# Kernel optimization log

Hardware: AMD Instinct MI355X
Metric: run time of the kernel (lower is better)

## Reference

```python
import jax, jax.numpy as jnp
import numpy as np


def silu(v):
    return v * jax.nn.sigmoid(v)


def setup_inputs() -> dict:
    key = jax.random.key(0)
    ks = jax.random.split(key, 9)
    B, L, d_model = 2, 2048, 1024
    expand, d_state, d_conv = 2, 16, 4
    d_inner = expand * d_model          # 2048
    dt_rank = (d_model + 15) // 16      # 64 (ceil(d_model/16))
    sc = 0.02
    s = lambda k, shape: (jax.random.normal(k, shape, jnp.float32) * sc)
    A_init = jnp.tile(jnp.arange(1, d_state + 1, dtype=jnp.float32), (d_inner, 1))
    return {
        "x": jax.random.normal(ks[0], (B, L, d_model), jnp.float32),
        "in_proj_w": s(ks[1], (2 * d_inner, d_model)),
        "conv_w": s(ks[2], (d_inner, 1, d_conv)),
        "conv_b": s(ks[3], (d_inner,)),
        "x_proj_w": s(ks[4], (dt_rank + 2 * d_state, d_inner)),
        "dt_proj_w": s(ks[5], (d_inner, dt_rank)),
        "dt_proj_b": s(ks[6], (d_inner,)),
        "A_log": jnp.log(A_init),
        "D": jnp.ones((d_inner,), jnp.float32),
        "out_proj_w": s(ks[7], (d_model, d_inner)),
    }


def _mamba(x, in_proj_w, conv_w, conv_b, x_proj_w, dt_proj_w, dt_proj_b, A_log, D, out_proj_w):
    Bsz, L, d_model = x.shape
    d_inner, _, d_conv = conv_w.shape
    d_state = A_log.shape[1]
    dt_rank = dt_proj_w.shape[1]

    # input projection -> [B, L, 2*d_inner], split into conv branch and gate
    xz = jnp.einsum('bld,ed->ble', x, in_proj_w)
    x_in, z = jnp.split(xz, 2, axis=-1)

    # causal depthwise conv1d over sequence
    xt = jnp.transpose(x_in, (0, 2, 1))                      # [B, d_inner, L]
    xt = jnp.pad(xt, ((0, 0), (0, 0), (d_conv - 1, 0)))
    xc = jax.lax.conv_general_dilated(
        xt, conv_w, window_strides=(1,), padding='VALID',
        dimension_numbers=('NCH', 'OIH', 'NCH'),
        feature_group_count=d_inner)
    xc = xc + conv_b[None, :, None]
    u = silu(jnp.transpose(xc, (0, 2, 1)))                   # [B, L, d_inner]

    # ssm parameter projections
    x_dbl = jnp.einsum('ble,fe->blf', u, x_proj_w)           # [B, L, dt_rank + 2*d_state]
    dt, B_ssm, C_ssm = jnp.split(x_dbl, [dt_rank, dt_rank + d_state], axis=-1)
    delta = jax.nn.softplus(jnp.einsum('blr,er->ble', dt, dt_proj_w) + dt_proj_b)  # [B,L,d_inner]
    A = -jnp.exp(A_log)                                       # [d_inner, d_state]

    # selective scan: h_t = exp(delta_t * A) * h_{t-1} + delta_t * u_t * B_t
    def step(h, inp):
        d_t, B_t, C_t, u_t = inp                              # [B,e],[B,n],[B,n],[B,e]
        dA = jnp.exp(d_t[..., None] * A)                      # [B, d_inner, d_state]
        h = dA * h + (d_t * u_t)[..., None] * B_t[:, None, :]
        y = jnp.einsum('ben,bn->be', h, C_t)
        return h, y

    h0 = jnp.zeros((Bsz, d_inner, d_state), x.dtype)
    scan_in = (jnp.swapaxes(delta, 0, 1), jnp.swapaxes(B_ssm, 0, 1),
               jnp.swapaxes(C_ssm, 0, 1), jnp.swapaxes(u, 0, 1))
    _, ys = jax.lax.scan(step, h0, scan_in)                   # ys: [L, B, d_inner]
    y = jnp.swapaxes(ys, 0, 1) + u * D                        # skip term D*u

    y = y * silu(z)                                           # gate
    return jnp.einsum('ble,de->bld', y, out_proj_w)


def reference(x, in_proj_w, conv_w, conv_b, x_proj_w, dt_proj_w, dt_proj_b, A_log, D, out_proj_w):
    # ResidualMamba: x + Mamba(x)
    return x + _mamba(x, in_proj_w, conv_w, conv_b, x_proj_w,
                      dt_proj_w, dt_proj_b, A_log, D, out_proj_w)
```

## Files before the change

kernel.cpp:

```cpp
#include <hip/hip_runtime.h>
#include <hip/hip_bf16.h>
#include <math.h>

typedef __bf16 bf16;
typedef __attribute__((ext_vector_type(8))) __bf16 bf16x8;
typedef __attribute__((ext_vector_type(4))) __bf16 bf16x4;
typedef __attribute__((ext_vector_type(4))) float  f32x4;

static constexpr int Bsz = 2, L = 2048, DM = 1024, DI = 2048, DS = 16, DTR = 64;
static constexpr int M   = Bsz * L;
static constexpr int NXZ = 2 * DI;
static constexpr int NXD = DTR + 2 * DS;
static constexpr int NC  = 32;
static constexpr int CL  = L / NC;
static constexpr int KS  = 8;
static constexpr float LOG2E = 1.4426950408889634f;

__device__ inline float ex2(float x) { return __builtin_amdgcn_exp2f(x); }

__device__ inline void gload_lds16(const void* g, void* l)
{
    __builtin_amdgcn_global_load_lds(
        (const __attribute__((address_space(1))) void*)g,
        (__attribute__((address_space(3))) void*)l, 16, 0, 0);
}

#define SBAR() { asm volatile("" ::: "memory"); __builtin_amdgcn_s_barrier(); asm volatile("" ::: "memory"); }
#define VMCNT4() asm volatile("s_waitcnt vmcnt(4)" ::: "memory")
#define VMCNT3() asm volatile("s_waitcnt vmcnt(3)" ::: "memory")
#define VMCNT0() asm volatile("s_waitcnt vmcnt(0)" ::: "memory")


static constexpr int C0 = M * DM / 4;
static constexpr int C1 = C0 + NXZ * DM / 4;
static constexpr int C2 = C1 + DM * DI / 4;
static constexpr int C3 = C2 + NXD * DI / 4;
static constexpr int C4 = C3 + DI * DTR / 4;

__global__ __launch_bounds__(256)
void cast_all(const float* __restrict__ s0, const float* __restrict__ s1,
              const float* __restrict__ s2, const float* __restrict__ s3,
              const float* __restrict__ s4,
              bf16* __restrict__ d0, bf16* __restrict__ d1,
              bf16* __restrict__ d2, bf16* __restrict__ d3,
              bf16* __restrict__ d4)
{
    const int i = blockIdx.x * 256 + threadIdx.x;
    const float* s; bf16* d; int off;
    if      (i < C0) { s = s0; d = d0; off = 0;  }
    else if (i < C1) { s = s1; d = d1; off = C0; }
    else if (i < C2) { s = s2; d = d2; off = C1; }
    else if (i < C3) { s = s3; d = d3; off = C2; }
    else             { s = s4; d = d4; off = C3; }
    const int j = i - off;
    float4 v = ((const float4*)s)[j];
    bf16x4 o = {(bf16)v.x, (bf16)v.y, (bf16)v.z, (bf16)v.w};
    ((bf16x4*)d)[j] = o;
}

static constexpr int GK  = DM;
static constexpr int GNT = GK / 64;

__device__ __forceinline__ void stage_half(const bf16* __restrict__ Gbase, int ld,
                                           int kbase, bf16* lds_slot, int tid, int wid)
{
    const int rl = tid >> 2;
    const int ks = ((((tid & 3) - ((tid >> 3) & 3)) & 3) << 3);
#pragma unroll
    for (int i = 0; i < 2; ++i)
        gload_lds16(Gbase + (size_t)(i * 128 + rl) * ld + kbase + ks,
                    lds_slot + i * 4096 + wid * 512);
}

template<int MH>
__device__ __forceinline__ void ldA4(const bf16* As, int abase, bf16x8 af[4])
{
#pragma unroll
    for (int mm = 0; mm < 4; ++mm)
        af[mm] = *(const bf16x8*)(As + abase + (MH * 4 + mm) * 512);
}

__device__ __forceinline__ void ldB4(const bf16* Bs, int bbase, bf16x8 bfr[4])
{
#pragma unroll
    for (int nn = 0; nn < 4; ++nn)
        bfr[nn] = *(const bf16x8*)(Bs + bbase + nn * 512);
}

template<int MH>
__device__ __forceinline__ void mfma16(f32x4 acc[8][4], const bf16x8 af[4],
                                       const bf16x8 bfr[4])
{
#pragma unroll
    for (int mm = 0; mm < 4; ++mm)
#pragma unroll
        for (int nn = 0; nn < 4; ++nn)
            acc[MH * 4 + mm][nn] = __builtin_amdgcn_mfma_f32_16x16x32_bf16(
                af[mm], bfr[nn], acc[MH * 4 + mm][nn], 0, 0, 0);
}

__global__ __launch_bounds__(512, 1)
void gemm256_inproj(const bf16* __restrict__ A, const bf16* __restrict__ Bw,
                    bf16* __restrict__ C)
{
    __shared__ __align__(16) bf16 Asl[4 * 8192];
    __shared__ __align__(16) bf16 Bsl[4 * 8192];

    const int tid  = threadIdx.x;
    const int wid  = tid >> 6;
    const int lane = tid & 63;
    const int wr   = wid >> 2;
    const int wc   = wid & 3;
    const int fr   = lane & 15;
    const int ko16 = lane >> 4;
    const int kx   = (((ko16 + ((fr >> 1) & 3)) & 3) << 3);

    const int bid = blockIdx.x;
    const int wg  = (bid & 7) * 32 + (bid >> 3);
    const int by  = wg >> 4, bx = wg & 15;
    const int row0 = by * 256, col0 = bx * 256;

    const bf16* Ablk = A  + (size_t)row0 * GK;
    const bf16* Bblk = Bw + (size_t)col0 * GK;

    const int abase = (wr * 128 + fr) * 32 + kx;
    const int bbase = (wc * 64 + fr) * 32 + kx;

    f32x4 acc[8][4] = {};
    bf16x8 af[4], bfr[4];

    stage_half(Ablk, GK, 0,       Asl + 0 * 8192, tid, wid);
    stage_half(Bblk, GK, 0,       Bsl + 0 * 8192, tid, wid);
    stage_half(Ablk, GK, 32,      Asl + 1 * 8192, tid, wid);
    stage_half(Bblk, GK, 32,      Bsl + 1 * 8192, tid, wid);
    stage_half(Ablk, GK, 64,      Asl + 2 * 8192, tid, wid);
    stage_half(Bblk, GK, 64,      Bsl + 2 * 8192, tid, wid);
    VMCNT4();
    SBAR();

    for (int t = 0; t < GNT; ++t) {
        const int sk0 = (2 * t) & 3, sk1 = (2 * t + 1) & 3;
        const bf16* As0 = Asl + sk0 * 8192;
        const bf16* As1 = Asl + sk1 * 8192;
        const bf16* Bs0 = Bsl + sk0 * 8192;
        const bf16* Bs1 = Bsl + sk1 * 8192;

        ldA4<0>(As0, abase, af);
        ldB4(Bs0, bbase, bfr);
        if (t + 1 < GNT)
            stage_half(Ablk, GK, (t + 1) * 64 + 32, Asl + ((2 * t + 3) & 3) * 8192, tid, wid);
        SBAR();
        __builtin_amdgcn_s_setprio(1);
        mfma16<0>(acc, af, bfr);
        __builtin_amdgcn_s_setprio(0);
        SBAR();

        ldA4<1>(As0, abase, af);
        if (t + 1 < GNT)
            stage_half(Bblk, GK, (t + 1) * 64 + 32, Bsl + ((2 * t + 3) & 3) * 8192, tid, wid);
        SBAR();
        __builtin_amdgcn_s_setprio(1);
        mfma16<1>(acc, af, bfr);
        __builtin_amdgcn_s_setprio(0);
        SBAR();

        ldA4<0>(As1, abase, af);
        ldB4(Bs1, bbase, bfr);
        if (t + 2 < GNT)
            stage_half(Ablk, GK, (t + 2) * 64, Asl + sk0 * 8192, tid, wid);
        SBAR();
        __builtin_amdgcn_s_setprio(1);
        mfma16<0>(acc, af, bfr);
        __builtin_amdgcn_s_setprio(0);
        SBAR();

        ldA4<1>(As1, abase, af);
        if (t + 2 < GNT)
            stage_half(Bblk, GK, (t + 2) * 64, Bsl + sk0 * 8192, tid, wid);
        SBAR();
        __builtin_amdgcn_s_setprio(1);
        mfma16<1>(acc, af, bfr);
        __builtin_amdgcn_s_setprio(0);
        if (t < GNT - 3) { VMCNT4(); } else { VMCNT0(); }
        SBAR();
    }

    const int r0 = row0 + wr * 128 + (ko16 << 2);
    const int c0 = col0 + wc * 64 + fr;
#pragma unroll
    for (int m = 0; m < 8; ++m)
#pragma unroll
        for (int n = 0; n < 4; ++n)
#pragma unroll
            for (int r = 0; r < 4; ++r)
                C[(size_t)(r0 + m * 16 + r) * NXZ + c0 + n * 16] = (bf16)acc[m][n][r];
}

__global__ __launch_bounds__(256)
void gemm_out(const bf16* __restrict__ A, const bf16* __restrict__ Bw,
              const float* __restrict__ res, float* __restrict__ Cout)
{
    __shared__ __align__(16) bf16 Asl[2][128 * 32];
    __shared__ __align__(16) bf16 Bsl[2][64 * 32];

    const int tid  = threadIdx.x;
    const int bid  = blockIdx.x;
    const int orig = (bid & 7) * 64 + (bid >> 3);
    const int bx   = orig & 15;
    const int by   = orig >> 4;
    const int row0 = by * 128, col0 = bx * 64;

    const int w    = tid >> 6;
    const int lane = tid & 63;
    const int wr   = w >> 1, wc = w & 1;
    const int fr   = lane & 15;
    const int ko   = (((lane >> 4) + ((fr >> 1) & 3)) & 3) << 3;

    f32x4 acc[4][2] = {};

    const int sr  = tid >> 2;
    const int ssk = ((((tid & 3) - ((tid >> 3) & 3)) & 3) << 3);
    const bf16* gA0 = A  + (size_t)(row0 + sr) * NXZ + ssk;
    const bf16* gA1 = A  + (size_t)(row0 + 64 + sr) * NXZ + ssk;
    const bf16* gB0 = Bw + (size_t)(col0 + sr) * DI + ssk;

#define STAGE_OUT(s, kk) do { \
        gload_lds16(gA0 + (kk), (char*)Asl[s] + w * 1024); \
        gload_lds16(gA1 + (kk), (char*)Asl[s] + 4096 + w * 1024); \
        gload_lds16(gB0 + (kk), (char*)Bsl[s] + w * 1024); } while (0)

    STAGE_OUT(0, 0);
    for (int k0 = 0; k0 < DI; k0 += 32) {
        const int cur = (k0 >> 5) & 1;
        if (k0 + 32 < DI) {
            STAGE_OUT(cur ^ 1, k0 + 32);
            VMCNT3();
        } else {
            VMCNT0();
        }
        SBAR();

        bf16x8 af[4], bfr[2];
#pragma unroll
        for (int m = 0; m < 4; ++m)
            af[m] = *(const bf16x8*)&Asl[cur][((wr << 6) + m * 16 + fr) * 32 + ko];
#pragma unroll
        for (int n = 0; n < 2; ++n)
            bfr[n] = *(const bf16x8*)&Bsl[cur][((wc << 5) + n * 16 + fr) * 32 + ko];
        __builtin_amdgcn_s_setprio(1);
#pragma unroll
        for (int m = 0; m < 4; ++m)
#pragma unroll
            for (int n = 0; n < 2; ++n)
                acc[m][n] = __builtin_amdgcn_mfma_f32_16x16x32_bf16(
                    af[m], bfr[n], acc[m][n], 0, 0, 0);
        __builtin_amdgcn_s_setprio(0);
        SBAR();
    }
#undef STAGE_OUT

    const int r0 = row0 + (wr << 6) + ((lane >> 4) << 2);
    const int c0 = col0 + (wc << 5) + fr;
#pragma unroll
    for (int m = 0; m < 4; ++m)
#pragma unroll
        for (int n = 0; n < 2; ++n)
#pragma unroll
            for (int r = 0; r < 4; ++r) {
                const int row = r0 + m * 16 + r;
                const int col = c0 + n * 16;
                Cout[(size_t)row * DM + col] =
                    acc[m][n][r] + res[(size_t)row * DM + col];
            }
}

template<int EPI>
__global__ __launch_bounds__(256)
void gemm_bf16(const bf16* __restrict__ A, const bf16* __restrict__ Bw,
               const float* __restrict__ bias, const float* __restrict__ res,
               void* __restrict__ Cout, int N, int K, int lda, int ldc)
{
    __shared__ __align__(16) bf16 Asl[128 * 32];
    __shared__ __align__(16) bf16 Bsl[128 * 32];

    const int tid  = threadIdx.x;
    const int row0 = blockIdx.y * 128;
    const int col0 = blockIdx.x * 128;
    const int w    = tid >> 6;
    const int lane = tid & 63;
    const int wr   = w >> 1, wc = w & 1;
    const int fr   = lane & 15;
    const int ko   = (((lane >> 4) + ((fr >> 1) & 3)) & 3) << 3;

    f32x4 acc[4][4] = {};

    const int sr  = tid >> 2;
    const int ssk = ((((tid & 3) - ((tid >> 3) & 3)) & 3) << 3);
    int brow0 = col0 + sr;       if (brow0 > N - 1) brow0 = N - 1;
    int brow1 = col0 + 64 + sr;  if (brow1 > N - 1) brow1 = N - 1;
    const bf16* gA0 = A  + (size_t)(row0 + sr) * lda + ssk;
    const bf16* gA1 = A  + (size_t)(row0 + 64 + sr) * lda + ssk;
    const bf16* gB0 = Bw + (size_t)brow0 * K + ssk;
    const bf16* gB1 = Bw + (size_t)brow1 * K + ssk;
    char* lA = (char*)Asl + w * 1024;
    char* lB = (char*)Bsl + w * 1024;

    for (int k0 = 0; k0 < K; k0 += 32) {
        gload_lds16(gA0 + k0, lA);
        gload_lds16(gA1 + k0, lA + 4096);
        gload_lds16(gB0 + k0, lB);
        gload_lds16(gB1 + k0, lB + 4096);
        __syncthreads();

        bf16x8 af[4], bfr[4];
#pragma unroll
        for (int m = 0; m < 4; ++m)
            af[m] = *(const bf16x8*)&Asl[((wr << 6) + m * 16 + fr) * 32 + ko];
#pragma unroll
        for (int n = 0; n < 4; ++n)
            bfr[n] = *(const bf16x8*)&Bsl[((wc << 6) + n * 16 + fr) * 32 + ko];
#pragma unroll
        for (int m = 0; m < 4; ++m)
#pragma unroll
            for (int n = 0; n < 4; ++n)
                acc[m][n] = __builtin_amdgcn_mfma_f32_16x16x32_bf16(
                    af[m], bfr[n], acc[m][n], 0, 0, 0);
        __syncthreads();
    }

    const int r0 = row0 + (wr << 6) + ((lane >> 4) << 2);
    const int c0 = col0 + (wc << 6) + fr;
#pragma unroll
    for (int m = 0; m < 4; ++m) {
#pragma unroll
        for (int n = 0; n < 4; ++n) {
            const int col = c0 + n * 16;
            if (col < N) {
#pragma unroll
                for (int r = 0; r < 4; ++r) {
                    const int row = r0 + m * 16 + r;
                    float v = acc[m][n][r];
                    if (EPI == 1) {
                        v += bias[col];
                        v = (v > 20.f) ? v : log1pf(expf(v));
                        ((bf16*)Cout)[(size_t)row * ldc + col] = (bf16)v;
                    } else {
                        ((bf16*)Cout)[(size_t)row * ldc + col] = (bf16)v;
                    }
                }
            }
        }
    }
}

__global__ __launch_bounds__(256)
void gemm_xproj(const bf16* __restrict__ A, const bf16* __restrict__ Bw,
                float* __restrict__ Cpart)
{
    __shared__ __align__(16) bf16 Asl[128 * 32];
    __shared__ __align__(16) bf16 Bsl[128 * 32];

    const int tid  = threadIdx.x;
    const int row0 = blockIdx.x * 128;
    const int kz   = blockIdx.y;
    const int kb   = kz * (2048 / KS);
    const int w    = tid >> 6;
    const int lane = tid & 63;
    const int wr   = w >> 1, wc = w & 1;
    const int fr   = lane & 15;
    const int ko   = (((lane >> 4) + ((fr >> 1) & 3)) & 3) << 3;

    f32x4 acc[4][4] = {};

    const int sr  = tid >> 2;
    const int ssk = ((((tid & 3) - ((tid >> 3) & 3)) & 3) << 3);
    int brow0 = sr;       if (brow0 > 95) brow0 = 95;
    int brow1 = 64 + sr;  if (brow1 > 95) brow1 = 95;
    const bf16* gA0 = A  + (size_t)(row0 + sr) * DI + kb + ssk;
    const bf16* gA1 = A  + (size_t)(row0 + 64 + sr) * DI + kb + ssk;
    const bf16* gB0 = Bw + (size_t)brow0 * DI + kb + ssk;
    const bf16* gB1 = Bw + (size_t)brow1 * DI + kb + ssk;
    char* lA = (char*)Asl + w * 1024;
    char* lB = (char*)Bsl + w * 1024;

    for (int k0 = 0; k0 < 2048 / KS; k0 += 32) {
        gload_lds16(gA0 + k0, lA);
        gload_lds16(gA1 + k0, lA + 4096);
        gload_lds16(gB0 + k0, lB);
        gload_lds16(gB1 + k0, lB + 4096);
        __syncthreads();

        bf16x8 af[4], bfr[4];
#pragma unroll
        for (int m = 0; m < 4; ++m)
            af[m] = *(const bf16x8*)&Asl[((wr << 6) + m * 16 + fr) * 32 + ko];
#pragma unroll
        for (int n = 0; n < 4; ++n)
            bfr[n] = *(const bf16x8*)&Bsl[((wc << 6) + n * 16 + fr) * 32 + ko];
#pragma unroll
        for (int m = 0; m < 4; ++m)
#pragma unroll
            for (int n = 0; n < 4; ++n)
                acc[m][n] = __builtin_amdgcn_mfma_f32_16x16x32_bf16(
                    af[m], bfr[n], acc[m][n], 0, 0, 0);
        __syncthreads();
    }

    const int r0 = (wr << 6) + ((lane >> 4) << 2);
    const int c0 = (wc << 6) + fr;
    float* Cp = Cpart + (size_t)kz * M * 96 + (size_t)row0 * 96;
#pragma unroll
    for (int m = 0; m < 4; ++m) {
#pragma unroll
        for (int n = 0; n < 4; ++n) {
            const int col = c0 + n * 16;
            if (col < 96) {
#pragma unroll
                for (int r = 0; r < 4; ++r)
                    Cp[(size_t)(r0 + m * 16 + r) * 96 + col] = acc[m][n][r];
            }
        }
    }
}

__global__ __launch_bounds__(256)
void reduce_xdbl(const float* __restrict__ part, bf16* __restrict__ xdb)
{
    const int i = blockIdx.x * 256 + threadIdx.x;
    if (i >= M * 96) return;
    float s = 0.f;
#pragma unroll
    for (int k = 0; k < KS; ++k) s += part[(size_t)k * M * 96 + i];
    xdb[i] = (bf16)s;
}

__global__ __launch_bounds__(256)
void conv_silu(const bf16* __restrict__ xzb, const float* __restrict__ cw,
               const float* __restrict__ cb, bf16* __restrict__ u)
{
    const int idx = blockIdx.x * 256 + threadIdx.x;
    const int e   = (idx & 255) * 8;
    const int m   = idx >> 8;
    const int l   = m & (L - 1);

    float wv[8][4];
#pragma unroll
    for (int c = 0; c < 8; ++c) {
        float4 t = *(const float4*)(cw + (size_t)(e + c) * 4);
        wv[c][0] = t.x; wv[c][1] = t.y; wv[c][2] = t.z; wv[c][3] = t.w;
    }
    float acc[8];
    {
        float4 b0 = *(const float4*)(cb + e);
        float4 b1 = *(const float4*)(cb + e + 4);
        acc[0] = b0.x; acc[1] = b0.y; acc[2] = b0.z; acc[3] = b0.w;
        acc[4] = b1.x; acc[5] = b1.y; acc[6] = b1.z; acc[7] = b1.w;
    }
#pragma unroll
    for (int k = 0; k < 4; ++k) {
        if (l + k - 3 >= 0) {
            bf16x8 xv = *(const bf16x8*)&xzb[(size_t)(m + k - 3) * NXZ + e];
#pragma unroll
            for (int c = 0; c < 8; ++c)
                acc[c] = fmaf((float)xv[c], wv[c][k], acc[c]);
        }
    }
    bf16x8 o;
#pragma unroll
    for (int c = 0; c < 8; ++c)
        o[c] = (bf16)(acc[c] / (1.f + __expf(-acc[c])));
    *(bf16x8*)&u[(size_t)m * DI + e] = o;
}

__global__ __launch_bounds__(256)
void scan_pass1(const bf16* __restrict__ xzb, const bf16* __restrict__ ub,
                const bf16* __restrict__ xdb, const float* __restrict__ A_log,
                float* __restrict__ Pend, float* __restrict__ Qend)
{
    __shared__ bf16 sD[CL][256];
    __shared__ bf16 sU[CL][256];
    __shared__ float Bs[CL][DS];
    const int tid = threadIdx.x;
    const int e0 = blockIdx.x * 256;
    const int e  = e0 + tid;
    const int c = blockIdx.y;
    const int b = blockIdx.z;
    const int l0 = c * CL;

#pragma unroll
    for (int it = 0; it < CL / 8; ++it) {
        const int r   = it * 8 + (tid >> 5);
        const int col = (tid & 31) * 8;
        *(bf16x8*)&sD[r][col] = *(const bf16x8*)&xzb[(size_t)(b * L + l0 + r) * NXZ + e0 + col];
        *(bf16x8*)&sU[r][col] = *(const bf16x8*)&ub [(size_t)(b * L + l0 + r) * DI  + e0 + col];
    }
#pragma unroll
    for (int it = 0; it < CL * DS / 256; ++it) {
        const int idx = it * 256 + tid;
        Bs[idx >> 4][idx & 15] =
            (float)xdb[(size_t)(b * L + l0 + (idx >> 4)) * NXD + DTR + (idx & 15)];
    }

    float A2[DS];
#pragma unroll
    for (int q = 0; q < 4; ++q) {
        float4 al = *(const float4*)(A_log + (size_t)e * DS + q * 4);
        A2[q * 4 + 0] = -__expf(al.x) * LOG2E;
        A2[q * 4 + 1] = -__expf(al.y) * LOG2E;
        A2[q * 4 + 2] = -__expf(al.z) * LOG2E;
        A2[q * 4 + 3] = -__expf(al.w) * LOG2E;
    }

    float h[DS];
#pragma unroll
    for (int n = 0; n < DS; ++n) h[n] = 0.f;
    float sumd = 0.f;

    __syncthreads();

#pragma unroll 4
    for (int t = 0; t < CL; ++t) {
        const float dv = (float)sD[t][tid];
        const float uv = (float)sU[t][tid];
        const float du = dv * uv;
        sumd += dv;
#pragma unroll
        for (int n = 0; n < DS; ++n) {
            const float a = ex2(dv * A2[n]);
            h[n] = fmaf(a, h[n], du * Bs[t][n]);
        }
    }

    const size_t o = ((size_t)(c * Bsz + b) * DI + e) * DS;
#pragma unroll
    for (int q = 0; q < 4; ++q) {
        f32x4 P = {ex2(A2[q*4] * sumd), ex2(A2[q*4+1] * sumd),
                   ex2(A2[q*4+2] * sumd), ex2(A2[q*4+3] * sumd)};
        *(f32x4*)(Pend + o + q * 4) = P;
        *(float4*)(Qend + o + q * 4) = make_float4(h[q*4], h[q*4+1], h[q*4+2], h[q*4+3]);
    }
}

__global__ __launch_bounds__(256)
void scan_pass2(const float* __restrict__ Pend, const float* __restrict__ Qend,
                float* __restrict__ H0)
{
    const int g = blockIdx.x * 256 + threadIdx.x;
    const int stride = Bsz * DI * DS;
    float P[NC], Q[NC];
#pragma unroll
    for (int c = 0; c < NC; ++c) {
        P[c] = Pend[(size_t)c * stride + g];
        Q[c] = Qend[(size_t)c * stride + g];
    }
    float h = 0.f;
#pragma unroll
    for (int c = 0; c < NC; ++c) {
        H0[(size_t)c * stride + g] = h;
        h = fmaf(P[c], h, Q[c]);
    }
}

__global__ __launch_bounds__(256)
void scan_pass3(bf16* __restrict__ xzb, const bf16* __restrict__ ub,
                const bf16* __restrict__ xdb, const float* __restrict__ A_log,
                const float* __restrict__ Dp, const float* __restrict__ H0)
{
    __shared__ bf16 sD[CL][256];
    __shared__ bf16 sU[CL][256];
    __shared__ float BCs[CL][2 * DS];
    const int tid = threadIdx.x;
    const int e0 = blockIdx.x * 256;
    const int e  = e0 + tid;
    const int c = blockIdx.y;
    const int b = blockIdx.z;
    const int l0 = c * CL;

#pragma unroll
    for (int it = 0; it < CL / 8; ++it) {
        const int r   = it * 8 + (tid >> 5);
        const int col = (tid & 31) * 8;
        const size_t grow = (size_t)(b * L + l0 + r);
        *(bf16x8*)&sD[r][col] = *(const bf16x8*)&xzb[grow * NXZ + e0 + col];
        *(bf16x8*)&sU[r][col] = *(const bf16x8*)&ub [grow * DI + e0 + col];
    }
#pragma unroll
    for (int it = 0; it < CL * 2 * DS / 256; ++it) {
        const int idx = it * 256 + tid;
        BCs[idx >> 5][idx & 31] =
            (float)xdb[(size_t)(b * L + l0 + (idx >> 5)) * NXD + DTR + (idx & 31)];
    }

    float A2[DS];
#pragma unroll
    for (int q = 0; q < 4; ++q) {
        float4 al = *(const float4*)(A_log + (size_t)e * DS + q * 4);
        A2[q * 4 + 0] = -__expf(al.x) * LOG2E;
        A2[q * 4 + 1] = -__expf(al.y) * LOG2E;
        A2[q * 4 + 2] = -__expf(al.z) * LOG2E;
        A2[q * 4 + 3] = -__expf(al.w) * LOG2E;
    }

    float h[DS];
    const size_t o = (size_t)c * (Bsz * DI * DS) + ((size_t)b * DI + e) * DS;
#pragma unroll
    for (int q = 0; q < 4; ++q) {
        float4 hv = *(const float4*)(H0 + o + q * 4);
        h[q*4] = hv.x; h[q*4+1] = hv.y; h[q*4+2] = hv.z; h[q*4+3] = hv.w;
    }
    const float Dval = Dp[e];

    __syncthreads();

#pragma unroll 4
    for (int t = 0; t < CL; ++t) {
        const float dv = (float)sD[t][tid];
        const float uv = (float)sU[t][tid];
        const float du = dv * uv;
        float y = 0.f;
#pragma unroll
        for (int n = 0; n < DS; ++n) {
            const float a = ex2(dv * A2[n]);
            h[n] = fmaf(a, h[n], du * BCs[t][n]);
            y = fmaf(h[n], BCs[t][DS + n], y);
        }
        sD[t][tid] = (bf16)(y + uv * Dval);
    }

    __syncthreads();
#pragma unroll
    for (int it = 0; it < CL / 8; ++it) {
        const int r   = it * 8 + (tid >> 5);
        const int col = (tid & 31) * 8;
        const size_t grow = (size_t)(b * L + l0 + r);
        bf16x8 zv = *(const bf16x8*)&xzb[grow * NXZ + DI + e0 + col];
        bf16x8 yv = *(bf16x8*)&sD[r][col];
        bf16x8 ov;
#pragma unroll
        for (int j = 0; j < 8; ++j) {
            const float z = (float)zv[j];
            ov[j] = (bf16)((float)yv[j] * (z / (1.f + __expf(-z))));
        }
        *(bf16x8*)&xzb[grow * NXZ + e0 + col] = ov;
    }
}

extern "C" void kernel_launch(void* const* d_in, const int* in_sizes, int n_in,
                              void* d_out, int out_size, void* d_ws, size_t ws_size,
                              hipStream_t stream)
{
    const float* x          = (const float*)d_in[0];
    const float* in_proj_w  = (const float*)d_in[1];
    const float* conv_w     = (const float*)d_in[2];
    const float* conv_b     = (const float*)d_in[3];
    const float* x_proj_w   = (const float*)d_in[4];
    const float* dt_proj_w  = (const float*)d_in[5];
    const float* dt_proj_b  = (const float*)d_in[6];
    const float* A_log      = (const float*)d_in[7];
    const float* Dp         = (const float*)d_in[8];
    const float* out_proj_w = (const float*)d_in[9];
    float* out = (float*)d_out;

    bf16* xzb   = (bf16*)d_ws;
    bf16* ub    = xzb   + (size_t)M * NXZ;
    bf16* xdb   = ub    + (size_t)M * DI;
    bf16* xb    = xdb   + (size_t)M * NXD;
    bf16* wbin  = xb    + (size_t)M * DM;
    bf16* wbout = wbin  + (size_t)NXZ * DM;
    bf16* wbxp  = wbout + (size_t)DM * DI;
    bf16* wbdt  = wbxp  + (size_t)NXD * DI;
    float* Pend = (float*)(wbdt + (size_t)DI * DTR);
    float* Qend = Pend + (size_t)NC * Bsz * DI * DS;
    float* H0   = Qend + (size_t)NC * Bsz * DI * DS;
    float* xpart = Pend;

    const dim3 blk(256);

    cast_all<<<dim3(C4 / 256), blk, 0, stream>>>(
        x, in_proj_w, out_proj_w, x_proj_w, dt_proj_w,
        xb, wbin, wbout, wbxp, wbdt);

    gemm256_inproj<<<dim3(256), dim3(512), 0, stream>>>(xb, wbin, xzb);

    conv_silu<<<dim3(M * (DI / 8) / 256), blk, 0, stream>>>(xzb, conv_w, conv_b, ub);

    gemm_xproj<<<dim3(M / 128, KS), blk, 0, stream>>>(ub, wbxp, xpart);
    reduce_xdbl<<<dim3(M * 96 / 256), blk, 0, stream>>>(xpart, xdb);

    gemm_bf16<1><<<dim3(DI / 128, M / 128), blk, 0, stream>>>(
        xdb, wbdt, dt_proj_b, nullptr, xzb, DI, DTR, NXD, NXZ);

    scan_pass1<<<dim3(DI / 256, NC, Bsz), blk, 0, stream>>>(xzb, ub, xdb, A_log, Pend, Qend);
    scan_pass2<<<dim3(Bsz * DI * DS / 256), blk, 0, stream>>>(Pend, Qend, H0);
    scan_pass3<<<dim3(DI / 256, NC, Bsz), blk, 0, stream>>>(xzb, ub, xdb, A_log, Dp, H0);

    gemm_out<<<dim3(512), blk, 0, stream>>>(xzb, wbout, x, out);
}
```

Measured before the change: 245.2 us.

## Fuse three scan passes into one persistent kernel with grid barriers

Merges the chunk-local scan, the cross-chunk prefix combine and the final scan into one 512-block kernel that uses atomic-counter grid barriers between the phases. The delta/u/B/C tiles stay in shared memory and A stays in registers across phases, so the second reload of these inputs and two kernel launches go away. The cost is two grid-wide spin barriers plus a memset. Correctness relies on all 512 blocks being co-resident, which the launch bounds of two blocks per CU are meant to guarantee; if they are not, the kernel deadlocks.

Measured after the change: 389.5 us. 58.8% more time.

```diff
diff --git a/kernel.cpp b/kernel.cpp
--- a/kernel.cpp
+++ b/kernel.cpp
@@ -30,6 +30,20 @@
 #define VMCNT3() asm volatile("s_waitcnt vmcnt(3)" ::: "memory")
 #define VMCNT0() asm volatile("s_waitcnt vmcnt(0)" ::: "memory")
 
+
+__device__ __forceinline__ void grid_bar(int* cnt, int target)
+{
+    __syncthreads();
+    if (threadIdx.x == 0) {
+        __threadfence();
+        atomicAdd(cnt, 1);
+        while (__hip_atomic_load(cnt, __ATOMIC_RELAXED,
+                                 __HIP_MEMORY_SCOPE_AGENT) < target)
+            __builtin_amdgcn_s_sleep(8);
+    }
+    __syncthreads();
+    __threadfence();
+}
 
 static constexpr int C0 = M * DM / 4;
 static constexpr int C1 = C0 + NXZ * DM / 4;
@@ -472,33 +486,39 @@
     *(bf16x8*)&u[(size_t)m * DI + e] = o;
 }
 
-__global__ __launch_bounds__(256)
-void scan_pass1(const bf16* __restrict__ xzb, const bf16* __restrict__ ub,
+__global__ __launch_bounds__(256, 2)
+void scan_fused(bf16* __restrict__ xzb, const bf16* __restrict__ ub,
                 const bf16* __restrict__ xdb, const float* __restrict__ A_log,
-                float* __restrict__ Pend, float* __restrict__ Qend)
+                const float* __restrict__ Dp,
+                float* __restrict__ Pend, float* __restrict__ Qend,
+                float* __restrict__ H0, int* __restrict__ bar)
 {
     __shared__ bf16 sD[CL][256];
     __shared__ bf16 sU[CL][256];
-    __shared__ float Bs[CL][DS];
+    __shared__ float BCs[CL][2 * DS];
     const int tid = threadIdx.x;
-    const int e0 = blockIdx.x * 256;
-    const int e  = e0 + tid;
-    const int c = blockIdx.y;
-    const int b = blockIdx.z;
-    const int l0 = c * CL;
+    const int bid = blockIdx.x;
+    const int eb  = bid & 7;
+    const int c   = (bid >> 3) & 31;
+    const int b   = bid >> 8;
+    const int e0  = eb * 256;
+    const int e   = e0 + tid;
+    const int l0  = c * CL;
+    const int stride = Bsz * DI * DS;
 
 #pragma unroll
     for (int it = 0; it < CL / 8; ++it) {
         const int r   = it * 8 + (tid >> 5);
         const int col = (tid & 31) * 8;
-        *(bf16x8*)&sD[r][col] = *(const bf16x8*)&xzb[(size_t)(b * L + l0 + r) * NXZ + e0 + col];
-        *(bf16x8*)&sU[r][col] = *(const bf16x8*)&ub [(size_t)(b * L + l0 + r) * DI  + e0 + col];
-    }
-#pragma unroll
-    for (int it = 0; it < CL * DS / 256; ++it) {
+        const size_t grow = (size_t)(b * L + l0 + r);
+        *(bf16x8*)&sD[r][col] = *(const bf16x8*)&xzb[grow * NXZ + e0 + col];
+        *(bf16x8*)&sU[r][col] = *(const bf16x8*)&ub [grow * DI + e0 + col];
+    }
+#pragma unroll
+    for (int it = 0; it < CL * 2 * DS / 256; ++it) {
         const int idx = it * 256 + tid;
-        Bs[idx >> 4][idx & 15] =
-            (float)xdb[(size_t)(b * L + l0 + (idx >> 4)) * NXD + DTR + (idx & 15)];
+        BCs[idx >> 5][idx & 31] =
+            (float)xdb[(size_t)(b * L + l0 + (idx >> 5)) * NXD + DTR + (idx & 31)];
     }
 
     float A2[DS];
@@ -527,90 +547,60 @@
 #pragma unroll
         for (int n = 0; n < DS; ++n) {
             const float a = ex2(dv * A2[n]);
-            h[n] = fmaf(a, h[n], du * Bs[t][n]);
-        }
-    }
-
-    const size_t o = ((size_t)(c * Bsz + b) * DI + e) * DS;
-#pragma unroll
-    for (int q = 0; q < 4; ++q) {
-        f32x4 P = {ex2(A2[q*4] * sumd), ex2(A2[q*4+1] * sumd),
-                   ex2(A2[q*4+2] * sumd), ex2(A2[q*4+3] * sumd)};
-        *(f32x4*)(Pend + o + q * 4) = P;
-        *(float4*)(Qend + o + q * 4) = make_float4(h[q*4], h[q*4+1], h[q*4+2], h[q*4+3]);
-    }
-}
-
-__global__ __launch_bounds__(256)
-void scan_pass2(const float* __restrict__ Pend, const float* __restrict__ Qend,
-                float* __restrict__ H0)
-{
-    const int g = blockIdx.x * 256 + threadIdx.x;
-    const int stride = Bsz * DI * DS;
-    float P[NC], Q[NC];
-#pragma unroll
-    for (int c = 0; c < NC; ++c) {
-        P[c] = Pend[(size_t)c * stride + g];
-        Q[c] = Qend[(size_t)c * stride + g];
-    }
-    float h = 0.f;
-#pragma unroll
-    for (int c = 0; c < NC; ++c) {
-        H0[(size_t)c * stride + g] = h;
-        h = fmaf(P[c], h, Q[c]);
-    }
-}
-
-__global__ __launch_bounds__(256)
-void scan_pass3(bf16* __restrict__ xzb, const bf16* __restrict__ ub,
-                const bf16* __restrict__ xdb, const float* __restrict__ A_log,
-                const float* __restrict__ Dp, const float* __restrict__ H0)
-{
-    __shared__ bf16 sD[CL][256];
-    __shared__ bf16 sU[CL][256];
-    __shared__ float BCs[CL][2 * DS];
-    const int tid = threadIdx.x;
-    const int e0 = blockIdx.x * 256;
-    const int e  = e0 + tid;
-    const int c = blockIdx.y;
-    const int b = blockIdx.z;
-    const int l0 = c * CL;
-
-#pragma unroll
-    for (int it = 0; it < CL / 8; ++it) {
-        const int r   = it * 8 + (tid >> 5);
-        const int col = (tid & 31) * 8;
-        const size_t grow = (size_t)(b * L + l0 + r);
-        *(bf16x8*)&sD[r][col] = *(const bf16x8*)&xzb[grow * NXZ + e0 + col];
-        *(bf16x8*)&sU[r][col] = *(const bf16x8*)&ub [grow * DI + e0 + col];
-    }
-#pragma unroll
-    for (int it = 0; it < CL * 2 * DS / 256; ++it) {
-        const int idx = it * 256 + tid;
-        BCs[idx >> 5][idx & 31] =
-            (float)xdb[(size_t)(b * L + l0 + (idx >> 5)) * NXD + DTR + (idx & 31)];
-    }
-
-    float A2[DS];
-#pragma unroll
-    for (int q = 0; q < 4; ++q) {
-        float4 al = *(const float4*)(A_log + (size_t)e * DS + q * 4);
-        A2[q * 4 + 0] = -__expf(al.x) * LOG2E;
-        A2[q * 4 + 1] = -__expf(al.y) * LOG2E;
-        A2[q * 4 + 2] = -__expf(al.z) * LOG2E;
-        A2[q * 4 + 3] = -__expf(al.w) * LOG2E;
-    }
-
-    float h[DS];
-    const size_t o = (size_t)c * (Bsz * DI * DS) + ((size_t)b * DI + e) * DS;
-#pragma unroll
-    for (int q = 0; q < 4; ++q) {
-        float4 hv = *(const float4*)(H0 + o + q * 4);
-        h[q*4] = hv.x; h[q*4+1] = hv.y; h[q*4+2] = hv.z; h[q*4+3] = hv.w;
+            h[n] = fmaf(a, h[n], du * BCs[t][n]);
+        }
+    }
+
+    {
+        const size_t o = (size_t)c * stride + ((size_t)b * DI + e) * DS;
+#pragma unroll
+        for (int q = 0; q < 4; ++q) {
+            f32x4 P = {ex2(A2[q*4] * sumd), ex2(A2[q*4+1] * sumd),
+                       ex2(A2[q*4+2] * sumd), ex2(A2[q*4+3] * sumd)};
+            *(f32x4*)(Pend + o + q * 4) = P;
+            *(float4*)(Qend + o + q * 4) = make_float4(h[q*4], h[q*4+1], h[q*4+2], h[q*4+3]);
+        }
+    }
+
+    grid_bar(bar, 512);
+
+    const int gtid = bid * 256 + tid;
+    if (gtid < stride) {
+        float Pv[16], Qv[16];
+        float hc = 0.f;
+#pragma unroll
+        for (int cc = 0; cc < 16; ++cc) {
+            Pv[cc] = Pend[(size_t)cc * stride + gtid];
+            Qv[cc] = Qend[(size_t)cc * stride + gtid];
+        }
+#pragma unroll
+        for (int cc = 0; cc < 16; ++cc) {
+            H0[(size_t)cc * stride + gtid] = hc;
+            hc = fmaf(Pv[cc], hc, Qv[cc]);
+        }
+#pragma unroll
+        for (int cc = 0; cc < 16; ++cc) {
+            Pv[cc] = Pend[(size_t)(16 + cc) * stride + gtid];
+            Qv[cc] = Qend[(size_t)(16 + cc) * stride + gtid];
+        }
+#pragma unroll
+        for (int cc = 0; cc < 16; ++cc) {
+            H0[(size_t)(16 + cc) * stride + gtid] = hc;
+            hc = fmaf(Pv[cc], hc, Qv[cc]);
+        }
+    }
+
+    grid_bar(bar + 1, 512);
+
+    {
+        const size_t o = (size_t)c * stride + ((size_t)b * DI + e) * DS;
+#pragma unroll
+        for (int q = 0; q < 4; ++q) {
+            float4 hv = *(const float4*)(H0 + o + q * 4);
+            h[q*4] = hv.x; h[q*4+1] = hv.y; h[q*4+2] = hv.z; h[q*4+3] = hv.w;
+        }
     }
     const float Dval = Dp[e];
-
-    __syncthreads();
 
 #pragma unroll 4
     for (int t = 0; t < CL; ++t) {
@@ -672,6 +662,7 @@
     float* Pend = (float*)(wbdt + (size_t)DI * DTR);
     float* Qend = Pend + (size_t)NC * Bsz * DI * DS;
     float* H0   = Qend + (size_t)NC * Bsz * DI * DS;
+    int*   bar  = (int*)(H0 + (size_t)NC * Bsz * DI * DS);
     float* xpart = Pend;
 
     const dim3 blk(256);
@@ -690,9 +681,9 @@
     gemm_bf16<1><<<dim3(DI / 128, M / 128), blk, 0, stream>>>(
         xdb, wbdt, dt_proj_b, nullptr, xzb, DI, DTR, NXD, NXZ);
 
-    scan_pass1<<<dim3(DI / 256, NC, Bsz), blk, 0, stream>>>(xzb, ub, xdb, A_log, Pend, Qend);
-    scan_pass2<<<dim3(Bsz * DI * DS / 256), blk, 0, stream>>>(Pend, Qend, H0);
-    scan_pass3<<<dim3(DI / 256, NC, Bsz), blk, 0, stream>>>(xzb, ub, xdb, A_log, Dp, H0);
+    hipMemsetAsync(bar, 0, 2 * sizeof(int), stream);
+    scan_fused<<<dim3(512), blk, 0, stream>>>(
+        xzb, ub, xdb, A_log, Dp, Pend, Qend, H0, bar);
 
     gemm_out<<<dim3(512), blk, 0, stream>>>(xzb, wbout, x, out);
 }
```

## Deepen async LDS prefetch to four stages in out-proj and x-proj GEMMs

Applied to the files above, without the earlier changes.

Replaces the double-buffered pipeline in gemm_out with a four-stage ring that keeps three tile loads in flight, using explicit vmcnt waits. Converts gemm_xproj from a synchronous load-then-compute loop to the same four-stage async global-to-LDS pipeline, and adds MFMA priority hints. The aim is to hide global memory latency behind MFMA work. In exchange LDS use grows, which may lower occupancy, and the hand-written wait counts must match the number of loads issued per stage.

Result: no change. 244.3 us, median of 2 (-0.4%).

```diff
diff --git a/kernel.cpp b/kernel.cpp
--- a/kernel.cpp
+++ b/kernel.cpp
@@ -26,9 +26,13 @@
 }
 
 #define SBAR() { asm volatile("" ::: "memory"); __builtin_amdgcn_s_barrier(); asm volatile("" ::: "memory"); }
-#define VMCNT4() asm volatile("s_waitcnt vmcnt(4)" ::: "memory")
-#define VMCNT3() asm volatile("s_waitcnt vmcnt(3)" ::: "memory")
-#define VMCNT0() asm volatile("s_waitcnt vmcnt(0)" ::: "memory")
+#define VMCNT12() asm volatile("s_waitcnt vmcnt(12)" ::: "memory")
+#define VMCNT9()  asm volatile("s_waitcnt vmcnt(9)" ::: "memory")
+#define VMCNT8()  asm volatile("s_waitcnt vmcnt(8)" ::: "memory")
+#define VMCNT6()  asm volatile("s_waitcnt vmcnt(6)" ::: "memory")
+#define VMCNT4()  asm volatile("s_waitcnt vmcnt(4)" ::: "memory")
+#define VMCNT3()  asm volatile("s_waitcnt vmcnt(3)" ::: "memory")
+#define VMCNT0()  asm volatile("s_waitcnt vmcnt(0)" ::: "memory")
 
 
 static constexpr int C0 = M * DM / 4;
@@ -200,8 +204,8 @@
 void gemm_out(const bf16* __restrict__ A, const bf16* __restrict__ Bw,
               const float* __restrict__ res, float* __restrict__ Cout)
 {
-    __shared__ __align__(16) bf16 Asl[2][128 * 32];
-    __shared__ __align__(16) bf16 Bsl[2][64 * 32];
+    __shared__ __align__(16) bf16 Asl[4][128 * 32];
+    __shared__ __align__(16) bf16 Bsl[4][64 * 32];
 
     const int tid  = threadIdx.x;
     const int bid  = blockIdx.x;
@@ -224,20 +228,22 @@
     const bf16* gA1 = A  + (size_t)(row0 + 64 + sr) * NXZ + ssk;
     const bf16* gB0 = Bw + (size_t)(col0 + sr) * DI + ssk;
 
+    const int NT = DI / 32;
+
 #define STAGE_OUT(s, kk) do { \
         gload_lds16(gA0 + (kk), (char*)Asl[s] + w * 1024); \
         gload_lds16(gA1 + (kk), (char*)Asl[s] + 4096 + w * 1024); \
         gload_lds16(gB0 + (kk), (char*)Bsl[s] + w * 1024); } while (0)
 
     STAGE_OUT(0, 0);
-    for (int k0 = 0; k0 < DI; k0 += 32) {
-        const int cur = (k0 >> 5) & 1;
-        if (k0 + 32 < DI) {
-            STAGE_OUT(cur ^ 1, k0 + 32);
-            VMCNT3();
-        } else {
-            VMCNT0();
-        }
+    STAGE_OUT(1, 32);
+    STAGE_OUT(2, 64);
+    for (int i = 0; i < NT; ++i) {
+        const int cur = i & 3;
+        if (i + 3 < NT)      { STAGE_OUT((i + 3) & 3, (i + 3) * 32); VMCNT9(); }
+        else if (i + 2 < NT) { VMCNT6(); }
+        else if (i + 1 < NT) { VMCNT3(); }
+        else                 { VMCNT0(); }
         SBAR();
 
         bf16x8 af[4], bfr[2];
@@ -357,8 +363,8 @@
 void gemm_xproj(const bf16* __restrict__ A, const bf16* __restrict__ Bw,
                 float* __restrict__ Cpart)
 {
-    __shared__ __align__(16) bf16 Asl[128 * 32];
-    __shared__ __align__(16) bf16 Bsl[128 * 32];
+    __shared__ __align__(16) bf16 Asl[4][128 * 32];
+    __shared__ __align__(16) bf16 Bsl[4][128 * 32];
 
     const int tid  = threadIdx.x;
     const int row0 = blockIdx.x * 128;
@@ -380,31 +386,44 @@
     const bf16* gA1 = A  + (size_t)(row0 + 64 + sr) * DI + kb + ssk;
     const bf16* gB0 = Bw + (size_t)brow0 * DI + kb + ssk;
     const bf16* gB1 = Bw + (size_t)brow1 * DI + kb + ssk;
-    char* lA = (char*)Asl + w * 1024;
-    char* lB = (char*)Bsl + w * 1024;
-
-    for (int k0 = 0; k0 < 2048 / KS; k0 += 32) {
-        gload_lds16(gA0 + k0, lA);
-        gload_lds16(gA1 + k0, lA + 4096);
-        gload_lds16(gB0 + k0, lB);
-        gload_lds16(gB1 + k0, lB + 4096);
-        __syncthreads();
+
+    const int NT = (2048 / KS) / 32;
+
+#define STAGE_XP(s, kk) do { \
+        gload_lds16(gA0 + (kk), (char*)Asl[s] + w * 1024); \
+        gload_lds16(gA1 + (kk), (char*)Asl[s] + 4096 + w * 1024); \
+        gload_lds16(gB0 + (kk), (char*)Bsl[s] + w * 1024); \
+        gload_lds16(gB1 + (kk), (char*)Bsl[s] + 4096 + w * 1024); } while (0)
+
+    STAGE_XP(0, 0);
+    STAGE_XP(1, 32);
+    STAGE_XP(2, 64);
+    for (int i = 0; i < NT; ++i) {
+        const int cur = i & 3;
+        if (i + 3 < NT)      { STAGE_XP((i + 3) & 3, (i + 3) * 32); VMCNT12(); }
+        else if (i + 2 < NT) { VMCNT8(); }
+        else if (i + 1 < NT) { VMCNT4(); }
+        else                 { VMCNT0(); }
+        SBAR();
 
         bf16x8 af[4], bfr[4];
 #pragma unroll
         for (int m = 0; m < 4; ++m)
-            af[m] = *(const bf16x8*)&Asl[((wr << 6) + m * 16 + fr) * 32 + ko];
+            af[m] = *(const bf16x8*)&Asl[cur][((wr << 6) + m * 16 + fr) * 32 + ko];
 #pragma unroll
         for (int n = 0; n < 4; ++n)
-            bfr[n] = *(const bf16x8*)&Bsl[((wc << 6) + n * 16 + fr) * 32 + ko];
+            bfr[n] = *(const bf16x8*)&Bsl[cur][((wc << 6) + n * 16 + fr) * 32 + ko];
+        __builtin_amdgcn_s_setprio(1);
 #pragma unroll
         for (int m = 0; m < 4; ++m)
 #pragma unroll
             for (int n = 0; n < 4; ++n)
                 acc[m][n] = __builtin_amdgcn_mfma_f32_16x16x32_bf16(
                     af[m], bfr[n], acc[m][n], 0, 0, 0);
-        __syncthreads();
-    }
+        __builtin_amdgcn_s_setprio(0);
+        SBAR();
+    }
+#undef STAGE_XP
 
     const int r0 = (wr << 6) + ((lane >> 4) << 2);
     const int c0 = (wc << 6) + fr;
```
